# Kernel optimization log

Hardware: AMD Instinct MI355X
Metric: run time of the kernel (lower is better)

## Reference

```python
import jax, jax.numpy as jnp
import numpy as np

LAYERS = 10
BLOCKS = 4
KERNEL = 2
# last block has LAYERS-1 layers, dilation doubles within each block
DILATIONS = [2 ** i for b in range(BLOCKS) for i in range(LAYERS if b < BLOCKS - 1 else LAYERS - 1)]
N_GATED = len(DILATIONS)  # 39


def conv1d(x, w, b, dilation=1):
    # x: [N, C_in, L], w: [C_out, C_in, K], valid (no) padding like the torch module
    y = jax.lax.conv_general_dilated(
        x, w, window_strides=(1,), padding='VALID',
        rhs_dilation=(dilation,), dimension_numbers=('NCH', 'OIH', 'NCH'))
    return y + b[None, :, None]


def setup_inputs() -> dict:
    key = jax.random.key(0)
    ks = jax.random.split(key, 11)
    w = lambda k, shape: jax.random.normal(k, shape, jnp.float32) * 0.05
    return {
        'x': jax.random.normal(ks[0], (8, 40, 8192), jnp.float32),
        'start_w': w(ks[1], (128, 40, 1)),
        'start_b': w(ks[2], (128,)),
        'dil_w': w(ks[3], (N_GATED, 256, 128, KERNEL)),  # 2*dilation_channels outputs
        'dil_b': w(ks[4], (N_GATED, 256)),
        'res_w': w(ks[5], (N_GATED, 128, 128, 1)),
        'res_b': w(ks[6], (N_GATED, 128)),
        'skip_w': w(ks[7], (N_GATED, 256, 128, 1)),
        'skip_b': w(ks[8], (N_GATED, 256)),
        'end_w': w(ks[9], (64, 256, 1)),
        'end_b': w(ks[10], (64,)),
    }


def reference(x, start_w, start_b, dil_w, dil_b, res_w, res_b, skip_w, skip_b, end_w, end_b):
    h = conv1d(x, start_w, start_b)
    skip = None
    for i, d in enumerate(DILATIONS):
        residual = h
        z = conv1d(h, dil_w[i], dil_b[i], dilation=d)  # [N, 2*dc, L-d]
        f, g = jnp.split(z, 2, axis=1)
        h = jnp.tanh(f) * jax.nn.sigmoid(g)
        s = conv1d(h, skip_w[i], skip_b[i])
        skip = s if skip is None else s + skip[:, :, -s.shape[2]:]
        h = conv1d(h, res_w[i], res_b[i])
        h = h + residual[:, :, -h.shape[2]:]
    out = conv1d(jax.nn.relu(skip), end_w, end_b)
    return out
```

## Files before the change

### kernel.cpp

```cpp
#include <hip/hip_runtime.h>

typedef __attribute__((ext_vector_type(8)))  short short8;
typedef __attribute__((ext_vector_type(4)))  float f32x4;
typedef __attribute__((ext_vector_type(16))) float f32x16;

#define L0    8192
#define LFIN  4612
#define PSKIP 3580

__device__ __forceinline__ unsigned short f2bf(float f) {
  unsigned u = __builtin_bit_cast(unsigned, f);
  u += 0x7fffu + ((u >> 16) & 1u);
  return (unsigned short)(u >> 16);
}
__device__ __forceinline__ float bf2f(unsigned short h) {
  return __builtin_bit_cast(float, (unsigned)h << 16);
}

__global__ __launch_bounds__(256) void wconv_kernel(
    const float* __restrict__ dw, const float* __restrict__ rw,
    const float* __restrict__ sw, const float* __restrict__ ew,
    const float* __restrict__ skb,
    unsigned short* __restrict__ Wd, unsigned short* __restrict__ Wr,
    unsigned short* __restrict__ Ws, unsigned short* __restrict__ We,
    float* __restrict__ SBS)
{
  int e = blockIdx.x * 256 + threadIdx.x;
  const int ND = 39*65536, NR = 39*16384, NS = 39*32768, NE = 16384;
  if (e < ND) {
    int i = e >> 16, r = e & 65535;
    int co = r >> 8, k = r & 255;
    int tap = k >> 7, ci = k & 127;
    Wd[e] = f2bf(dw[(((size_t)i*256 + co)*128 + ci)*2 + tap]);
  } else if ((e -= ND) < NR) {
    Wr[e] = f2bf(rw[e]);
  } else if ((e -= NR) < NS) {
    Ws[e] = f2bf(sw[e]);
  } else if ((e -= NS) < NE) {
    We[e] = f2bf(ew[e]);
  } else if ((e -= NE) < 256) {
    float s = 0.f;
    for (int i = 0; i < 39; ++i) s += skb[i*256 + e];
    SBS[e] = s;
  }
}

__global__ __launch_bounds__(256) void start_kernel(
    const float* __restrict__ x, const float* __restrict__ w,
    const float* __restrict__ b, unsigned short* __restrict__ H)
{
  __shared__ float xs[40][64];
  __shared__ float wl[128*41];
  const int tid = threadIdx.x;
  const int n = blockIdx.y;
  const int p0 = blockIdx.x * 64;

  for (int e = tid; e < 40*64; e += 256) {
    int ci = e >> 6, t = e & 63;
    xs[ci][t] = x[((size_t)n*40 + ci)*L0 + p0 + t];
  }
  for (int e = tid; e < 128*40; e += 256)
    wl[(e/40)*41 + (e%40)] = w[e];
  __syncthreads();

  const int c  = tid & 127;
  const int ph = tid >> 7;
  const float bias = b[c];
  #pragma unroll 4
  for (int k = 0; k < 32; ++k) {
    int p = ph + 2*k;
    float acc = bias;
    #pragma unroll
    for (int ci = 0; ci < 40; ++ci)
      acc = fmaf(wl[c*41 + ci], xs[ci][p], acc);
    H[((size_t)n*L0 + p0 + p)*128 + c] = f2bf(acc);
  }
}

__device__ __forceinline__ void gate_write(char* Gl, const float* __restrict__ dbl,
    const f32x16& af, const f32x16& ag, int p, int w, int hi)
{
  #pragma unroll
  for (int q = 0; q < 4; ++q) {
    int rbase = 8*q + 4*hi;
    const float4 bf4 = *(const float4*)&dbl[32*w + rbase];
    const float4 bg4 = *(const float4*)&dbl[128 + 32*w + rbase];
    const float bfv[4] = {bf4.x, bf4.y, bf4.z, bf4.w};
    const float bgv[4] = {bg4.x, bg4.y, bg4.z, bg4.w};
    unsigned short gs[4];
    #pragma unroll
    for (int r = 0; r < 4; ++r) {
      float fv = af[4*q + r] + bfv[r];
      float gg = ag[4*q + r] + bgv[r];
      float th = 2.f * __builtin_amdgcn_rcpf(1.f + __expf(-2.f * fv)) - 1.f;
      float sg = __builtin_amdgcn_rcpf(1.f + __expf(-gg));
      gs[r] = f2bf(th * sg);
    }
    ushort4 gv; gv.x = gs[0]; gv.y = gs[1]; gv.z = gs[2]; gv.w = gs[3];
    int byte = ((p << 8) + ((32*w + rbase) << 1)) ^ ((p & 7) << 4);
    *(ushort4*)(Gl + byte) = gv;
  }
}

__device__ __forceinline__ void res_writeback(char* Hl, const float* __restrict__ rbl,
    const f32x16& racc, int sl, int w, int hi)
{
  #pragma unroll
  for (int q = 0; q < 4; ++q) {
    int co = 32*w + 8*q + 4*hi;
    const float4 rb4 = *(const float4*)&rbl[co];
    int hbyte = ((sl << 8) + (co << 1)) ^ ((sl & 7) << 4);
    ushort4 hv = *(const ushort4*)(Hl + hbyte);
    ushort4 hb;
    hb.x = f2bf(racc[4*q]   + rb4.x + bf2f(hv.x));
    hb.y = f2bf(racc[4*q+1] + rb4.y + bf2f(hv.y));
    hb.z = f2bf(racc[4*q+2] + rb4.z + bf2f(hv.z));
    hb.w = f2bf(racc[4*q+3] + rb4.w + bf2f(hv.w));
    *(ushort4*)(Hl + hbyte) = hb;
  }
}

__global__ __launch_bounds__(256, 1) void group_mfma(
    const unsigned short* __restrict__ Hin, unsigned short* __restrict__ Hout,
    float* __restrict__ SK,
    const unsigned short* __restrict__ Wd, const float* __restrict__ dilb,
    const unsigned short* __restrict__ Wr, const float* __restrict__ resb,
    const unsigned short* __restrict__ Ws,
    int s, int NL, int i0, int accum, int writeH)
{
  __shared__ __align__(16) unsigned short Hl[96*128];
  __shared__ __align__(16) unsigned short Gl[96*128];

  const int tid = threadIdx.x;
  const int lb = blockIdx.x;
  const int n = lb & 7;
  const int u = lb >> 3;
  const int r = (s == 1) ? 0 : (u & 31);
  const int t = (s == 1) ? u : (u >> 5);
  const int mbase = t*64 - 32;

  const int w = tid >> 6, lane = tid & 63;
  const int ln = lane & 31, hi = lane >> 5;

  const unsigned short* __restrict__ Hb = Hin + (size_t)n * L0 * 128;

  #pragma unroll
  for (int it = 0; it < 6; ++it) {
    int e = it*256 + tid;
    int c8 = (e & 15) << 3;
    int j  = e >> 4;
    int gp = r + s * (mbase + j);
    if (gp < 0) gp = 0;
    short8 v = *(const short8*)&Hb[(size_t)gp * 128 + c8];
    *(short8*)((char*)Hl + (((j << 8) + (c8 << 1)) ^ ((j & 7) << 4))) = v;
  }
  __syncthreads();

  const f32x16 fz16 = {0.f};
  f32x16 sk00 = fz16, sk01 = fz16, sk10 = fz16, sk11 = fz16;
  const bool doSkip = (r + s*(t*64 + 63)) >= PSKIP;

  #pragma unroll 1
  for (int l = 0; l < NL; ++l) {
    const int i = i0 + l;
    const int dil = 1 << l;
    const unsigned short* __restrict__ Wdl = Wd + (size_t)l*65536;
    const float* dbl = dilb + l*256;

    const int r1_0 = ln,      r1_1 = 32 + ln,  r1_2 = 64 + ln;
    int rc_0 = r1_0 - dil; if (rc_0 < 0) rc_0 = 0;
    const int rc_1 = r1_1 - dil, rc_2 = r1_2 - dil;
    f32x16 af0 = fz16, af1 = fz16, af2 = fz16;
    f32x16 ag0 = fz16, ag1 = fz16, ag2 = fz16;
    #pragma unroll
    for (int ks = 0; ks < 16; ++ks) {
      int colb = (ks & 7)*32 + hi*16;
      short8 Af = *(const short8*)&Wdl[(size_t)(32*w + ln)*256 + ks*16 + hi*8];
      short8 Ag = *(const short8*)&Wdl[(size_t)(128 + 32*w + ln)*256 + ks*16 + hi*8];
      int row0 = (ks < 8) ? rc_0 : r1_0;
      int row1 = (ks < 8) ? rc_1 : r1_1;
      int row2 = (ks < 8) ? rc_2 : r1_2;
      short8 B0 = *(const short8*)((const char*)Hl + ((row0 << 8) + (colb ^ ((row0 & 7) << 4))));
      short8 B1 = *(const short8*)((const char*)Hl + ((row1 << 8) + (colb ^ ((row1 & 7) << 4))));
      short8 B2 = *(const short8*)((const char*)Hl + ((row2 << 8) + (colb ^ ((row2 & 7) << 4))));
      af0 = __builtin_amdgcn_mfma_f32_32x32x16_bf16(Af, B0, af0, 0, 0, 0);
      ag0 = __builtin_amdgcn_mfma_f32_32x32x16_bf16(Ag, B0, ag0, 0, 0, 0);
      af1 = __builtin_amdgcn_mfma_f32_32x32x16_bf16(Af, B1, af1, 0, 0, 0);
      ag1 = __builtin_amdgcn_mfma_f32_32x32x16_bf16(Ag, B1, ag1, 0, 0, 0);
      af2 = __builtin_amdgcn_mfma_f32_32x32x16_bf16(Af, B2, af2, 0, 0, 0);
      ag2 = __builtin_amdgcn_mfma_f32_32x32x16_bf16(Ag, B2, ag2, 0, 0, 0);
    }
    gate_write((char*)Gl, dbl, af0, ag0, r1_0, w, hi);
    gate_write((char*)Gl, dbl, af1, ag1, r1_1, w, hi);
    gate_write((char*)Gl, dbl, af2, ag2, r1_2, w, hi);
    __syncthreads();

    if (doSkip) {
      const unsigned short* __restrict__ Wsl = Ws + (size_t)l*32768;
      const int rB0 = 32 + ln, rB1 = 64 + ln;
      #pragma unroll
      for (int ks = 0; ks < 8; ++ks) {
        int colb = ks*32 + hi*16;
        short8 A0 = *(const short8*)&Wsl[(size_t)(32*w + ln)*128 + ks*16 + hi*8];
        short8 A1 = *(const short8*)&Wsl[(size_t)(128 + 32*w + ln)*128 + ks*16 + hi*8];
        short8 B0 = *(const short8*)((const char*)Gl +
                      ((rB0 << 8) + (colb ^ ((rB0 & 7) << 4))));
        short8 B1 = *(const short8*)((const char*)Gl +
                      ((rB1 << 8) + (colb ^ ((rB1 & 7) << 4))));
        sk00 = __builtin_amdgcn_mfma_f32_32x32x16_bf16(A0, B0, sk00, 0, 0, 0);
        sk01 = __builtin_amdgcn_mfma_f32_32x32x16_bf16(A0, B1, sk01, 0, 0, 0);
        sk10 = __builtin_amdgcn_mfma_f32_32x32x16_bf16(A1, B0, sk10, 0, 0, 0);
        sk11 = __builtin_amdgcn_mfma_f32_32x32x16_bf16(A1, B1, sk11, 0, 0, 0);
      }
    }

    if (i < 38) {
      const unsigned short* __restrict__ Wrl = Wr + (size_t)l*16384;
      const float* rbl = resb + l*128;
      f32x16 rk0 = fz16, rk1 = fz16, rk2 = fz16;
      #pragma unroll
      for (int ks = 0; ks < 8; ++ks) {
        int colb = ks*32 + hi*16;
        short8 A = *(const short8*)&Wrl[(size_t)(32*w + ln)*128 + ks*16 + hi*8];
        short8 B0 = *(const short8*)((const char*)Gl +
                      ((r1_0 << 8) + (colb ^ ((r1_0 & 7) << 4))));
        short8 B1 = *(const short8*)((const char*)Gl +
                      ((r1_1 << 8) + (colb ^ ((r1_1 & 7) << 4))));
        short8 B2 = *(const short8*)((const char*)Gl +
                      ((r1_2 << 8) + (colb ^ ((r1_2 & 7) << 4))));
        rk0 = __builtin_amdgcn_mfma_f32_32x32x16_bf16(A, B0, rk0, 0, 0, 0);
        rk1 = __builtin_amdgcn_mfma_f32_32x32x16_bf16(A, B1, rk1, 0, 0, 0);
        rk2 = __builtin_amdgcn_mfma_f32_32x32x16_bf16(A, B2, rk2, 0, 0, 0);
      }
      if (l < NL-1)
        res_writeback((char*)Hl, rbl, rk0, r1_0, w, hi);
      res_writeback((char*)Hl, rbl, rk1, r1_1, w, hi);
      res_writeback((char*)Hl, rbl, rk2, r1_2, w, hi);
    }
    __syncthreads();
  }

  if (writeH) {
    unsigned short* __restrict__ Ho = Hout + (size_t)n * L0 * 128;
    #pragma unroll
    for (int it = 0; it < 4; ++it) {
      int e = it*256 + tid;
      int c8 = (e & 15) << 3;
      int j  = 32 + (e >> 4);
      int gp = r + s * (mbase + j);
      short8 v = *(const short8*)((const char*)Hl +
                   (((j << 8) + (c8 << 1)) ^ ((j & 7) << 4)));
      *(short8*)&Ho[(size_t)gp * 128 + c8] = v;
    }
  }

  if (doSkip) {
    float* SKn = SK + (size_t)n * LFIN * 256;
    #pragma unroll
    for (int nb = 0; nb < 2; ++nb) {
      int sl = 32 + nb*32 + ln;
      int p = r + s * (mbase + sl);
      if (p >= PSKIP) {
        int pi = p - PSKIP;
        #pragma unroll
        for (int q = 0; q < 4; ++q) {
          const f32x16& a0 = nb ? sk01 : sk00;
          const f32x16& a1 = nb ? sk11 : sk10;
          {
            int co = 32*w + 8*q + 4*hi;
            float* dst = &SKn[(size_t)pi * 256 + co];
            float4 v = make_float4(a0[4*q], a0[4*q+1], a0[4*q+2], a0[4*q+3]);
            if (accum) {
              float4 o = *(const float4*)dst;
              v.x += o.x; v.y += o.y; v.z += o.z; v.w += o.w;
            }
            *(float4*)dst = v;
          }
          {
            int co = 32*w + 128 + 8*q + 4*hi;
            float* dst = &SKn[(size_t)pi * 256 + co];
            float4 v = make_float4(a1[4*q], a1[4*q+1], a1[4*q+2], a1[4*q+3]);
            if (accum) {
              float4 o = *(const float4*)dst;
              v.x += o.x; v.y += o.y; v.z += o.z; v.w += o.w;
            }
            *(float4*)dst = v;
          }
        }
      }
    }
  }
}

__global__ __launch_bounds__(256) void end_mfma(
    const float* __restrict__ SK, const unsigned short* __restrict__ We,
    const float* __restrict__ SBS, const float* __restrict__ eb,
    float* __restrict__ out)
{
  __shared__ unsigned short sl[64*256];
  const int tid = threadIdx.x;
  const int n = blockIdx.y;
  const int p0 = blockIdx.x * 64;
  const float* __restrict__ SKn = SK + (size_t)n * LFIN * 256;

  #pragma unroll
  for (int it = 0; it < 16; ++it) {
    int e = it * 256 + tid;
    int c4 = (e & 63) << 2;
    int p  = e >> 6;
    int gp = p0 + p; if (gp > LFIN - 1) gp = LFIN - 1;
    float4 v = *(const float4*)&SKn[(size_t)gp * 256 + c4];
    float4 s4 = *(const float4*)&SBS[c4];
    ushort4 h;
    h.x = f2bf(fmaxf(v.x + s4.x, 0.f)); h.y = f2bf(fmaxf(v.y + s4.y, 0.f));
    h.z = f2bf(fmaxf(v.z + s4.z, 0.f)); h.w = f2bf(fmaxf(v.w + s4.w, 0.f));
    int byte = ((p << 9) + (c4 << 1)) ^ ((p & 7) << 4);
    *(ushort4*)((char*)sl + byte) = h;
  }
  __syncthreads();

  const int w  = tid >> 6, lane = tid & 63;
  const int lr = lane & 15, lg = lane >> 4;
  const f32x4 fz = {0.f, 0.f, 0.f, 0.f};
  f32x4 acc[4] = {fz, fz, fz, fz};

  #pragma unroll
  for (int ks = 0; ks < 8; ++ks) {
    short8 A = *(const short8*)&We[(size_t)(16*w + lr) * 256 + ks*32 + lg*8];
    #pragma unroll
    for (int nb = 0; nb < 4; ++nb) {
      int p = nb * 16 + lr;
      int byte = ((p << 9) + ((ks*32 + lg*8) << 1)) ^ ((p & 7) << 4);
      short8 B = *(const short8*)((const char*)sl + byte);
      acc[nb] = __builtin_amdgcn_mfma_f32_16x16x32_bf16(A, B, acc[nb], 0, 0, 0);
    }
  }
  #pragma unroll
  for (int nb = 0; nb < 4; ++nb) {
    int p = p0 + nb*16 + lr;
    if (p < LFIN) {
      #pragma unroll
      for (int r = 0; r < 4; ++r) {
        int co = 16*w + lg*4 + r;
        out[((size_t)n*64 + co) * LFIN + p] = acc[nb][r] + eb[co];
      }
    }
  }
}

extern "C" void kernel_launch(void* const* d_in, const int* in_sizes, int n_in,
                              void* d_out, int out_size, void* d_ws, size_t ws_size,
                              hipStream_t stream)
{
  const float* x      = (const float*)d_in[0];
  const float* startw = (const float*)d_in[1];
  const float* startb = (const float*)d_in[2];
  const float* dilw   = (const float*)d_in[3];
  const float* dilb   = (const float*)d_in[4];
  const float* resw   = (const float*)d_in[5];
  const float* resb   = (const float*)d_in[6];
  const float* skipw  = (const float*)d_in[7];
  const float* skipb  = (const float*)d_in[8];
  const float* endw   = (const float*)d_in[9];
  const float* endb   = (const float*)d_in[10];

  unsigned short* H0 = (unsigned short*)d_ws;
  unsigned short* H1 = H0 + (size_t)8*L0*128;
  float* SK = (float*)(H1 + (size_t)8*L0*128);
  unsigned short* Wd = (unsigned short*)(SK + (size_t)8*LFIN*256);
  unsigned short* Wr = Wd + (size_t)39*65536;
  unsigned short* Ws = Wr + (size_t)39*16384;
  unsigned short* We = Ws + (size_t)39*32768;
  float* SBS = (float*)(We + 16384);

  const int total = 39*65536 + 39*16384 + 39*32768 + 16384 + 256;
  wconv_kernel<<<(total + 255)/256, 256, 0, stream>>>(dilw, resw, skipw, endw, skipb,
                                                      Wd, Wr, Ws, We, SBS);
  start_kernel<<<dim3(L0/64, 8), 256, 0, stream>>>(x, startw, startb, H0);

  static const int GI0[8] = {0, 5, 10, 15, 20, 25, 30, 35};
  static const int GNL[8] = {5, 5, 5, 5, 5, 5, 5, 4};
  static const int GS [8] = {1, 32, 1, 32, 1, 32, 1, 32};

  unsigned short* bufs[2] = {H0, H1};
  for (int g = 0; g < 8; ++g) {
    int i0 = GI0[g];
    group_mfma<<<dim3(1024), 256, 0, stream>>>(
        bufs[g & 1], bufs[(g & 1) ^ 1], SK,
        Wd + (size_t)i0*65536, dilb + (size_t)i0*256,
        Wr + (size_t)i0*16384, resb + (size_t)i0*128,
        Ws + (size_t)i0*32768,
        GS[g], GNL[g], i0, g ? 1 : 0, (g < 7) ? 1 : 0);
  }

  end_mfma<<<dim3((LFIN + 63)/64, 8), 256, 0, stream>>>(SK, We, SBS, endb, (float*)d_out);
}
```

Before: 1.620 ms.

## Halve group tile to 32 outputs, raise occupancy and widen LDS swizzle

Each group block now computes 32 output positions with a 32-row halo instead of 64, so it needs half the LDS and accumulators. The launch bound is raised to 3 blocks per CU and the grid doubled to 2048 blocks, aiming to hide latency and the syncthreads stalls. The XOR swizzle now uses 16 row bits instead of 8 to cut LDS bank conflicts. In exchange the halo fraction grows from a third to half of each tile, so redundant dilated-conv work and input loads per output go up.

```diff
diff --git a/kernel.cpp b/kernel.cpp
--- a/kernel.cpp
+++ b/kernel.cpp
@@ -7,6 +7,8 @@
 #define L0    8192
 #define LFIN  4612
 #define PSKIP 3580
+
+#define SWZ(rr) (((rr) & 15) << 4)
 
 __device__ __forceinline__ unsigned short f2bf(float f) {
   unsigned u = __builtin_bit_cast(unsigned, f);
@@ -97,7 +99,7 @@
       gs[r] = f2bf(th * sg);
     }
     ushort4 gv; gv.x = gs[0]; gv.y = gs[1]; gv.z = gs[2]; gv.w = gs[3];
-    int byte = ((p << 8) + ((32*w + rbase) << 1)) ^ ((p & 7) << 4);
+    int byte = ((p << 8) + ((32*w + rbase) << 1)) ^ SWZ(p);
     *(ushort4*)(Gl + byte) = gv;
   }
 }
@@ -109,7 +111,7 @@
   for (int q = 0; q < 4; ++q) {
     int co = 32*w + 8*q + 4*hi;
     const float4 rb4 = *(const float4*)&rbl[co];
-    int hbyte = ((sl << 8) + (co << 1)) ^ ((sl & 7) << 4);
+    int hbyte = ((sl << 8) + (co << 1)) ^ SWZ(sl);
     ushort4 hv = *(const ushort4*)(Hl + hbyte);
     ushort4 hb;
     hb.x = f2bf(racc[4*q]   + rb4.x + bf2f(hv.x));
@@ -120,7 +122,7 @@
   }
 }
 
-__global__ __launch_bounds__(256, 1) void group_mfma(
+__global__ __launch_bounds__(256, 3) void group_mfma(
     const unsigned short* __restrict__ Hin, unsigned short* __restrict__ Hout,
     float* __restrict__ SK,
     const unsigned short* __restrict__ Wd, const float* __restrict__ dilb,
@@ -128,8 +130,8 @@
     const unsigned short* __restrict__ Ws,
     int s, int NL, int i0, int accum, int writeH)
 {
-  __shared__ __align__(16) unsigned short Hl[96*128];
-  __shared__ __align__(16) unsigned short Gl[96*128];
+  __shared__ __align__(16) unsigned short Hl[64*128];
+  __shared__ __align__(16) unsigned short Gl[64*128];
 
   const int tid = threadIdx.x;
   const int lb = blockIdx.x;
@@ -137,7 +139,7 @@
   const int u = lb >> 3;
   const int r = (s == 1) ? 0 : (u & 31);
   const int t = (s == 1) ? u : (u >> 5);
-  const int mbase = t*64 - 32;
+  const int mbase = t*32 - 32;
 
   const int w = tid >> 6, lane = tid & 63;
   const int ln = lane & 31, hi = lane >> 5;
@@ -145,20 +147,20 @@
   const unsigned short* __restrict__ Hb = Hin + (size_t)n * L0 * 128;
 
   #pragma unroll
-  for (int it = 0; it < 6; ++it) {
+  for (int it = 0; it < 4; ++it) {
     int e = it*256 + tid;
     int c8 = (e & 15) << 3;
     int j  = e >> 4;
     int gp = r + s * (mbase + j);
     if (gp < 0) gp = 0;
     short8 v = *(const short8*)&Hb[(size_t)gp * 128 + c8];
-    *(short8*)((char*)Hl + (((j << 8) + (c8 << 1)) ^ ((j & 7) << 4))) = v;
+    *(short8*)((char*)Hl + (((j << 8) + (c8 << 1)) ^ SWZ(j))) = v;
   }
   __syncthreads();
 
   const f32x16 fz16 = {0.f};
-  f32x16 sk00 = fz16, sk01 = fz16, sk10 = fz16, sk11 = fz16;
-  const bool doSkip = (r + s*(t*64 + 63)) >= PSKIP;
+  f32x16 sk0 = fz16, sk1 = fz16;
+  const bool doSkip = (r + s*(t*32 + 31)) >= PSKIP;
 
   #pragma unroll 1
   for (int l = 0; l < NL; ++l) {
@@ -167,11 +169,10 @@
     const unsigned short* __restrict__ Wdl = Wd + (size_t)l*65536;
     const float* dbl = dilb + l*256;
 
-    const int r1_0 = ln,      r1_1 = 32 + ln,  r1_2 = 64 + ln;
+    const int r1_0 = ln, r1_1 = 32 + ln;
     int rc_0 = r1_0 - dil; if (rc_0 < 0) rc_0 = 0;
-    const int rc_1 = r1_1 - dil, rc_2 = r1_2 - dil;
-    f32x16 af0 = fz16, af1 = fz16, af2 = fz16;
-    f32x16 ag0 = fz16, ag1 = fz16, ag2 = fz16;
+    const int rc_1 = r1_1 - dil;
+    f32x16 af0 = fz16, af1 = fz16, ag0 = fz16, ag1 = fz16;
     #pragma unroll
     for (int ks = 0; ks < 16; ++ks) {
       int colb = (ks & 7)*32 + hi*16;
@@ -179,63 +180,50 @@
       short8 Ag = *(const short8*)&Wdl[(size_t)(128 + 32*w + ln)*256 + ks*16 + hi*8];
       int row0 = (ks < 8) ? rc_0 : r1_0;
       int row1 = (ks < 8) ? rc_1 : r1_1;
-      int row2 = (ks < 8) ? rc_2 : r1_2;
-      short8 B0 = *(const short8*)((const char*)Hl + ((row0 << 8) + (colb ^ ((row0 & 7) << 4))));
-      short8 B1 = *(const short8*)((const char*)Hl + ((row1 << 8) + (colb ^ ((row1 & 7) << 4))));
-      short8 B2 = *(const short8*)((const char*)Hl + ((row2 << 8) + (colb ^ ((row2 & 7) << 4))));
+      short8 B0 = *(const short8*)((const char*)Hl + ((row0 << 8) + (colb ^ SWZ(row0))));
+      short8 B1 = *(const short8*)((const char*)Hl + ((row1 << 8) + (colb ^ SWZ(row1))));
       af0 = __builtin_amdgcn_mfma_f32_32x32x16_bf16(Af, B0, af0, 0, 0, 0);
       ag0 = __builtin_amdgcn_mfma_f32_32x32x16_bf16(Ag, B0, ag0, 0, 0, 0);
       af1 = __builtin_amdgcn_mfma_f32_32x32x16_bf16(Af, B1, af1, 0, 0, 0);
       ag1 = __builtin_amdgcn_mfma_f32_32x32x16_bf16(Ag, B1, ag1, 0, 0, 0);
-      af2 = __builtin_amdgcn_mfma_f32_32x32x16_bf16(Af, B2, af2, 0, 0, 0);
-      ag2 = __builtin_amdgcn_mfma_f32_32x32x16_bf16(Ag, B2, ag2, 0, 0, 0);
     }
     gate_write((char*)Gl, dbl, af0, ag0, r1_0, w, hi);
     gate_write((char*)Gl, dbl, af1, ag1, r1_1, w, hi);
-    gate_write((char*)Gl, dbl, af2, ag2, r1_2, w, hi);
     __syncthreads();
 
     if (doSkip) {
       const unsigned short* __restrict__ Wsl = Ws + (size_t)l*32768;
-      const int rB0 = 32 + ln, rB1 = 64 + ln;
+      const int rB = 32 + ln;
       #pragma unroll
       for (int ks = 0; ks < 8; ++ks) {
         int colb = ks*32 + hi*16;
         short8 A0 = *(const short8*)&Wsl[(size_t)(32*w + ln)*128 + ks*16 + hi*8];
         short8 A1 = *(const short8*)&Wsl[(size_t)(128 + 32*w + ln)*128 + ks*16 + hi*8];
-        short8 B0 = *(const short8*)((const char*)Gl +
-                      ((rB0 << 8) + (colb ^ ((rB0 & 7) << 4))));
-        short8 B1 = *(const short8*)((const char*)Gl +
-                      ((rB1 << 8) + (colb ^ ((rB1 & 7) << 4))));
-        sk00 = __builtin_amdgcn_mfma_f32_32x32x16_bf16(A0, B0, sk00, 0, 0, 0);
-        sk01 = __builtin_amdgcn_mfma_f32_32x32x16_bf16(A0, B1, sk01, 0, 0, 0);
-        sk10 = __builtin_amdgcn_mfma_f32_32x32x16_bf16(A1, B0, sk10, 0, 0, 0);
-        sk11 = __builtin_amdgcn_mfma_f32_32x32x16_bf16(A1, B1, sk11, 0, 0, 0);
+        short8 B = *(const short8*)((const char*)Gl +
+                     ((rB << 8) + (colb ^ SWZ(rB))));
+        sk0 = __builtin_amdgcn_mfma_f32_32x32x16_bf16(A0, B, sk0, 0, 0, 0);
+        sk1 = __builtin_amdgcn_mfma_f32_32x32x16_bf16(A1, B, sk1, 0, 0, 0);
       }
     }
 
     if (i < 38) {
       const unsigned short* __restrict__ Wrl = Wr + (size_t)l*16384;
       const float* rbl = resb + l*128;
-      f32x16 rk0 = fz16, rk1 = fz16, rk2 = fz16;
+      f32x16 rk0 = fz16, rk1 = fz16;
       #pragma unroll
       for (int ks = 0; ks < 8; ++ks) {
         int colb = ks*32 + hi*16;
         short8 A = *(const short8*)&Wrl[(size_t)(32*w + ln)*128 + ks*16 + hi*8];
         short8 B0 = *(const short8*)((const char*)Gl +
-                      ((r1_0 << 8) + (colb ^ ((r1_0 & 7) << 4))));
+                      ((r1_0 << 8) + (colb ^ SWZ(r1_0))));
         short8 B1 = *(const short8*)((const char*)Gl +
-                      ((r1_1 << 8) + (colb ^ ((r1_1 & 7) << 4))));
-        short8 B2 = *(const short8*)((const char*)Gl +
-                      ((r1_2 << 8) + (colb ^ ((r1_2 & 7) << 4))));
+                      ((r1_1 << 8) + (colb ^ SWZ(r1_1))));
         rk0 = __builtin_amdgcn_mfma_f32_32x32x16_bf16(A, B0, rk0, 0, 0, 0);
         rk1 = __builtin_amdgcn_mfma_f32_32x32x16_bf16(A, B1, rk1, 0, 0, 0);
-        rk2 = __builtin_amdgcn_mfma_f32_32x32x16_bf16(A, B2, rk2, 0, 0, 0);
       }
       if (l < NL-1)
         res_writeback((char*)Hl, rbl, rk0, r1_0, w, hi);
       res_writeback((char*)Hl, rbl, rk1, r1_1, w, hi);
-      res_writeback((char*)Hl, rbl, rk2, r1_2, w, hi);
     }
     __syncthreads();
   }
@@ -243,49 +231,44 @@
   if (writeH) {
     unsigned short* __restrict__ Ho = Hout + (size_t)n * L0 * 128;
     #pragma unroll
-    for (int it = 0; it < 4; ++it) {
+    for (int it = 0; it < 2; ++it) {
       int e = it*256 + tid;
       int c8 = (e & 15) << 3;
       int j  = 32 + (e >> 4);
       int gp = r + s * (mbase + j);
       short8 v = *(const short8*)((const char*)Hl +
-                   (((j << 8) + (c8 << 1)) ^ ((j & 7) << 4)));
+                   (((j << 8) + (c8 << 1)) ^ SWZ(j)));
       *(short8*)&Ho[(size_t)gp * 128 + c8] = v;
     }
   }
 
   if (doSkip) {
     float* SKn = SK + (size_t)n * LFIN * 256;
-    #pragma unroll
-    for (int nb = 0; nb < 2; ++nb) {
-      int sl = 32 + nb*32 + ln;
-      int p = r + s * (mbase + sl);
-      if (p >= PSKIP) {
-        int pi = p - PSKIP;
-        #pragma unroll
-        for (int q = 0; q < 4; ++q) {
-          const f32x16& a0 = nb ? sk01 : sk00;
-          const f32x16& a1 = nb ? sk11 : sk10;
-          {
-            int co = 32*w + 8*q + 4*hi;
-            float* dst = &SKn[(size_t)pi * 256 + co];
-            float4 v = make_float4(a0[4*q], a0[4*q+1], a0[4*q+2], a0[4*q+3]);
-            if (accum) {
-              float4 o = *(const float4*)dst;
-              v.x += o.x; v.y += o.y; v.z += o.z; v.w += o.w;
-            }
-            *(float4*)dst = v;
+    int sl = 32 + ln;
+    int p = r + s * (mbase + sl);
+    if (p >= PSKIP) {
+      int pi = p - PSKIP;
+      #pragma unroll
+      for (int q = 0; q < 4; ++q) {
+        {
+          int co = 32*w + 8*q + 4*hi;
+          float* dst = &SKn[(size_t)pi * 256 + co];
+          float4 v = make_float4(sk0[4*q], sk0[4*q+1], sk0[4*q+2], sk0[4*q+3]);
+          if (accum) {
+            float4 o = *(const float4*)dst;
+            v.x += o.x; v.y += o.y; v.z += o.z; v.w += o.w;
           }
-          {
-            int co = 32*w + 128 + 8*q + 4*hi;
-            float* dst = &SKn[(size_t)pi * 256 + co];
-            float4 v = make_float4(a1[4*q], a1[4*q+1], a1[4*q+2], a1[4*q+3]);
-            if (accum) {
-              float4 o = *(const float4*)dst;
-              v.x += o.x; v.y += o.y; v.z += o.z; v.w += o.w;
-            }
-            *(float4*)dst = v;
+          *(float4*)dst = v;
+        }
+        {
+          int co = 32*w + 128 + 8*q + 4*hi;
+          float* dst = &SKn[(size_t)pi * 256 + co];
+          float4 v = make_float4(sk1[4*q], sk1[4*q+1], sk1[4*q+2], sk1[4*q+3]);
+          if (accum) {
+            float4 o = *(const float4*)dst;
+            v.x += o.x; v.y += o.y; v.z += o.z; v.w += o.w;
           }
+          *(float4*)dst = v;
         }
       }
     }
@@ -385,7 +368,7 @@
   unsigned short* bufs[2] = {H0, H1};
   for (int g = 0; g < 8; ++g) {
     int i0 = GI0[g];
-    group_mfma<<<dim3(1024), 256, 0, stream>>>(
+    group_mfma<<<dim3(2048), 256, 0, stream>>>(
         bufs[g & 1], bufs[(g & 1) ^ 1], SK,
         Wd + (size_t)i0*65536, dilb + (size_t)i0*256,
         Wr + (size_t)i0*16384, resb + (size_t)i0*128,
```

Measured after the change: 2.172 ms. 34.1% more time.
